# Optimization experiments

Measured on AMD Instinct MI355X. Metric: run time of the kernel, lower is better.

The kernel has to match this reference:

```python
import jax, jax.numpy as jnp
import numpy as np

B, C, L = 8, 512, 2048


def setup_inputs() -> dict:
    key = jax.random.key(0)
    ks = jax.random.split(key, 7)
    s = 1.0 / np.sqrt(C)
    return {
        "x": jax.random.normal(ks[0], (B, C, L), dtype=jnp.float32),
        "Wq": jax.random.normal(ks[1], (C, C), dtype=jnp.float32) * s,
        "bq": jax.random.normal(ks[2], (C,), dtype=jnp.float32) * s,
        "Wk": jax.random.normal(ks[3], (C, C), dtype=jnp.float32) * s,
        "bk": jax.random.normal(ks[4], (C,), dtype=jnp.float32) * s,
        "Wv": jax.random.normal(ks[5], (C, C), dtype=jnp.float32) * s,
        "bv": jax.random.normal(ks[6], (C,), dtype=jnp.float32) * s,
    }


def reference(x, Wq, bq, Wk, bk, Wv, bv):
    # Conv1d(kernel_size=1) == per-position linear: [C_out, C_in] @ x[b,:,l]
    q = jnp.einsum('oi,bil->bol', Wq, x) + bq[None, :, None]  # [B, C, L]
    k = jnp.einsum('oi,bil->bol', Wk, x) + bk[None, :, None]
    v = jnp.einsum('oi,bil->bol', Wv, x) + bv[None, :, None]
    scale = 1.0 / jnp.sqrt(jnp.asarray(x.shape[1], dtype=x.dtype))
    # scores[b, l, m] = sum_c q[b,c,l] * k[b,c,m] / sqrt(C)
    scores = jnp.einsum('bcl,bcm->blm', q, k) * scale  # [B, L, L]
    attn = jax.nn.softmax(scores, axis=-1)
    # out[b, c, l] = sum_m v[b,c,m] * attn[b,l,m]   (== bmm(V, attn^T))
    return jnp.einsum('bcm,blm->bcl', v, attn)  # [B, C, L]
```

## Files before the change

### kernel.cpp

```cpp
#include <hip/hip_runtime.h>
#include <hip/hip_bf16.h>
#include <math.h>

#define B 8
#define C 512
#define L 2048

using bf16x8 = __bf16 __attribute__((ext_vector_type(8)));
using f32x4  = float __attribute__((ext_vector_type(4)));

#define MFMA(a, b, c) __builtin_amdgcn_mfma_f32_16x16x32_bf16((a), (b), (c), 0, 0, 0)
#define SC2 0.06375872f
#define SH2 -17.312340f

__device__ __forceinline__ unsigned short f2bf(float f) {
    unsigned int u; __builtin_memcpy(&u, &f, 4);
    u += 0x7FFF + ((u >> 16) & 1);
    return (unsigned short)(u >> 16);
}
__device__ __forceinline__ void load_lds16(const unsigned short* g, unsigned short* l) {
    __builtin_amdgcn_global_load_lds(
        (const __attribute__((address_space(1))) unsigned int*)g,
        (__attribute__((address_space(3))) unsigned int*)l, 16, 0, 0);
}

template<int MODE, int KDIM>
__device__ __forceinline__ void gemm_core(
    const unsigned short* __restrict__ A,
    const unsigned short* __restrict__ Bm,
    unsigned short* As, unsigned short* Bs,
    void* __restrict__ OutV, int ldo,
    float* __restrict__ ep)
{
    const int t = threadIdx.x;
    const int wave = t >> 6, lane = t & 63;
    const int ll = t & 15, quad = (t >> 4) & 3;
    const int lr = lane >> 2, chunk = lane & 3;
    const int wm = (wave & 1) * 64, wn = (wave >> 1) * 64;

    const unsigned short* gA0 = A  + (size_t)(wave * 32 + lr) * KDIM + chunk * 8;
    const unsigned short* gB0 = Bm + (size_t)(wave * 32 + lr) * KDIM + chunk * 8;
    unsigned short* lA0 = As + (wave * 32) * 32;
    unsigned short* lB0 = Bs + (wave * 32) * 32;
    const int P1 = 128 * 32;

    f32x4 acc[4][4];
#pragma unroll
    for (int i = 0; i < 4; ++i)
#pragma unroll
        for (int j = 0; j < 4; ++j) acc[i][j] = (f32x4){0.f, 0.f, 0.f, 0.f};

#pragma unroll 1
    for (int k0 = 0; k0 < KDIM; k0 += 64) {
        __syncthreads();
        load_lds16(gA0 + k0, lA0);
        load_lds16(gA0 + (size_t)16 * KDIM + k0, lA0 + 16 * 32);
        load_lds16(gA0 + k0 + 32, lA0 + P1);
        load_lds16(gA0 + (size_t)16 * KDIM + k0 + 32, lA0 + P1 + 16 * 32);
        load_lds16(gB0 + k0, lB0);
        load_lds16(gB0 + (size_t)16 * KDIM + k0, lB0 + 16 * 32);
        load_lds16(gB0 + k0 + 32, lB0 + P1);
        load_lds16(gB0 + (size_t)16 * KDIM + k0 + 32, lB0 + P1 + 16 * 32);
        __syncthreads();

#pragma unroll
        for (int p = 0; p < 2; ++p) {
            bf16x8 af[4], bf[4];
#pragma unroll
            for (int mi = 0; mi < 4; ++mi)
                af[mi] = *(const bf16x8*)&As[p * P1 + (wm + mi * 16 + ll) * 32 + quad * 8];
#pragma unroll
            for (int ni = 0; ni < 4; ++ni)
                bf[ni] = *(const bf16x8*)&Bs[p * P1 + (wn + ni * 16 + ll) * 32 + quad * 8];
#pragma unroll
            for (int mi = 0; mi < 4; ++mi)
#pragma unroll
                for (int ni = 0; ni < 4; ++ni)
                    acc[mi][ni] = MFMA(af[mi], bf[ni], acc[mi][ni]);
        }
    }

#pragma unroll
    for (int mi = 0; mi < 4; ++mi)
#pragma unroll
        for (int ni = 0; ni < 4; ++ni) {
            const int col = wn + ni * 16 + ll;
            float epc = 0.f;
            if (MODE == 0) epc = ep[col];
            if (MODE == 3) epc = 1.0f / ep[col];
#pragma unroll
            for (int r = 0; r < 4; ++r) {
                const int row = wm + mi * 16 + quad * 4 + r;
                float v = acc[mi][ni][r];
                if (MODE == 0)      v += epc;
                else if (MODE == 1) v += ep[row];
                else                v *= epc;
                if (MODE == 3)
                    ((float*)OutV)[(size_t)row * ldo + col] = v;
                else
                    ((unsigned short*)OutV)[(size_t)row * ldo + col] = f2bf(v);
            }
        }
}

__global__ __launch_bounds__(256) void prep(
    const float* __restrict__ x, const float* __restrict__ Wq,
    const float* __restrict__ Wk, const float* __restrict__ Wv,
    unsigned short* __restrict__ xt, unsigned short* __restrict__ o,
    float* __restrict__ rsum)
{
    __shared__ float tile[64][69];
    const int t = threadIdx.x;
    const int flat = blockIdx.x + 32 * (blockIdx.y + 8 * blockIdx.z);

    if (flat < 768) {
        if (flat < 16) {
            float4 z = make_float4(0.f, 0.f, 0.f, 0.f);
            *(float4*)(rsum + (flat * 256 + t) * 4) = z;
        }
        const int i = (flat * 256 + t) * 4;
        const int which = i >> 18;
        const int off = i & 0x3FFFF;
        const float* src = (which == 0) ? Wq : (which == 1) ? Wk : Wv;
        float4 v = *(const float4*)(src + off);
        union { unsigned short h[4]; uint2 u; } pk;
        pk.h[0] = f2bf(v.x); pk.h[1] = f2bf(v.y); pk.h[2] = f2bf(v.z); pk.h[3] = f2bf(v.w);
        *(uint2*)(o + i) = pk.u;
    }

    const int b = blockIdx.z, l0 = blockIdx.x * 64, c0 = blockIdx.y * 64;
    const int lx = t & 15, cy = t >> 4;
    const float* xb = x + (size_t)b * C * L;
#pragma unroll
    for (int p = 0; p < 4; ++p) {
        float4 v = *(const float4*)(xb + (size_t)(c0 + p * 16 + cy) * L + l0 + lx * 4);
        tile[p * 16 + cy][lx * 4 + 0] = v.x;
        tile[p * 16 + cy][lx * 4 + 1] = v.y;
        tile[p * 16 + cy][lx * 4 + 2] = v.z;
        tile[p * 16 + cy][lx * 4 + 3] = v.w;
    }
    __syncthreads();
    const int ocl = t & 15, ot = t >> 4;
    unsigned short* xtb = xt + (size_t)b * L * C;
#pragma unroll
    for (int p = 0; p < 4; ++p) {
        int ol = p * 16 + ot;
        union { unsigned short h[4]; uint2 u; } pk;
#pragma unroll
        for (int i = 0; i < 4; ++i) pk.h[i] = f2bf(tile[ocl * 4 + i][ol]);
        *(uint2*)(xtb + (size_t)(l0 + ol) * C + c0 + ocl * 4) = pk.u;
    }
}

__global__ __launch_bounds__(256) void qkv_gemm(
    const unsigned short* __restrict__ xt, const unsigned short* __restrict__ Wb,
    const float* __restrict__ bq, const float* __restrict__ bk,
    const float* __restrict__ bv,
    unsigned short* __restrict__ Qt, unsigned short* __restrict__ Kt,
    unsigned short* __restrict__ Vv)
{
    __shared__ unsigned short As[2 * 128 * 32], Bs[2 * 128 * 32];
    const int id = blockIdx.x;
    const int b = id & 7, r = id >> 3;
    const int which = r >> 6, tt = r & 63;
    const unsigned short* xtb = xt + (size_t)b * L * C;
    if (which < 2) {
        const int m0 = (tt & 15) * 128, n0 = (tt >> 4) * 128;
        const unsigned short* A  = xtb + (size_t)m0 * C;
        const unsigned short* Bm = Wb + (size_t)which * C * C + (size_t)n0 * C;
        unsigned short* Out = (which ? Kt : Qt) + (size_t)b * L * C
                              + (size_t)m0 * C + n0;
        gemm_core<0, C>(A, Bm, As, Bs, Out, C,
                        const_cast<float*>((which ? bk : bq) + n0));
    } else {
        const int m0 = (tt & 3) * 128, n0 = (tt >> 2) * 128;
        const unsigned short* A  = Wb + (size_t)2 * C * C + (size_t)m0 * C;
        const unsigned short* Bm = xtb + (size_t)n0 * C;
        unsigned short* Out = Vv + (size_t)b * C * L + (size_t)m0 * L + n0;
        gemm_core<1, C>(A, Bm, As, Bs, Out, L, const_cast<float*>(bv + m0));
    }
}

__global__ __launch_bounds__(512, 4) void sc_exp3(
    const unsigned short* __restrict__ Qt, const unsigned short* __restrict__ Kt,
    unsigned short* __restrict__ P, float* __restrict__ rsum,
    int hoff, int qrows, int mshift)
{
    __shared__ unsigned short As[256 * 64];
    __shared__ unsigned short Bs[128 * 64];
    constexpr int KD = C;

    const int id = blockIdx.x;
    const int b = id & 7, rr = id >> 3;
    const int m0 = (rr & ((1 << mshift) - 1)) * 256, n0 = (rr >> mshift) * 128;
    const unsigned short* A  = Qt + (size_t)b * L * C + (size_t)(hoff + m0) * C;
    const unsigned short* Bm = Kt + (size_t)b * L * C + (size_t)n0 * C;
    unsigned short* Out = P + (size_t)b * qrows * L + (size_t)m0 * L + n0;
    float* ep = rsum + (size_t)b * L + hoff + m0;

    const int t = threadIdx.x;
    const int wave = t >> 6;
    const int ll = t & 15, quad = (t >> 4) & 3;
    const int wm = (wave & 3) * 64, wn = (wave >> 2) * 64;

    const int r0 = t >> 3;
    const int swz = ((t & 7) ^ (r0 & 7)) * 8;
    const unsigned short* gA = A  + (size_t)r0 * KD + swz;
    const unsigned short* gB = Bm + (size_t)r0 * KD + swz;
    unsigned short* lA = As + wave * 512;
    unsigned short* lB = Bs + wave * 512;
    const int sw8 = ll & 7;

    f32x4 acc[4][4];
#pragma unroll
    for (int i = 0; i < 4; ++i)
#pragma unroll
        for (int j = 0; j < 4; ++j) acc[i][j] = (f32x4){0.f, 0.f, 0.f, 0.f};

#pragma unroll 1
    for (int k0 = 0; k0 < KD; k0 += 64) {
        __syncthreads();
        load_lds16(gA + k0,                     lA);
        load_lds16(gA + (size_t)64  * KD + k0,  lA + 64 * 64);
        load_lds16(gA + (size_t)128 * KD + k0,  lA + 128 * 64);
        load_lds16(gA + (size_t)192 * KD + k0,  lA + 192 * 64);
        load_lds16(gB + k0,                     lB);
        load_lds16(gB + (size_t)64  * KD + k0,  lB + 64 * 64);
        __syncthreads();

#pragma unroll
        for (int p = 0; p < 2; ++p) {
            bf16x8 af[4], bf[4];
#pragma unroll
            for (int mi = 0; mi < 4; ++mi)
                af[mi] = *(const bf16x8*)&As[(wm + mi * 16 + ll) * 64
                                             + ((p * 4 + quad) ^ sw8) * 8];
#pragma unroll
            for (int ni = 0; ni < 4; ++ni)
                bf[ni] = *(const bf16x8*)&Bs[(wn + ni * 16 + ll) * 64
                                             + ((p * 4 + quad) ^ sw8) * 8];
#pragma unroll
            for (int mi = 0; mi < 4; ++mi)
#pragma unroll
                for (int ni = 0; ni < 4; ++ni)
                    acc[mi][ni] = MFMA(af[mi], bf[ni], acc[mi][ni]);
        }
    }

    float rpart[4][4];
#pragma unroll
    for (int mi = 0; mi < 4; ++mi)
#pragma unroll
        for (int r = 0; r < 4; ++r) rpart[mi][r] = 0.f;

#pragma unroll
    for (int mi = 0; mi < 4; ++mi)
#pragma unroll
        for (int ni = 0; ni < 4; ++ni) {
            const int col = wn + ni * 16 + ll;
#pragma unroll
            for (int r = 0; r < 4; ++r) {
                const int row = wm + mi * 16 + quad * 4 + r;
                float v = exp2f(fmaf(acc[mi][ni][r], SC2, SH2));
                rpart[mi][r] += v;
                Out[(size_t)row * L + col] = f2bf(v);
            }
        }
#pragma unroll
    for (int mi = 0; mi < 4; ++mi)
#pragma unroll
        for (int r = 0; r < 4; ++r) {
            float s = rpart[mi][r];
            s += __shfl_xor(s, 1, 64);
            s += __shfl_xor(s, 2, 64);
            s += __shfl_xor(s, 4, 64);
            s += __shfl_xor(s, 8, 64);
            if (ll == 0) atomicAdd(ep + wm + mi * 16 + quad * 4 + r, s);
        }
}

__global__ __launch_bounds__(512, 4) void pv_gemm2(
    const unsigned short* __restrict__ Vv, const unsigned short* __restrict__ P,
    const float* __restrict__ rsum, float* __restrict__ out)
{
    __shared__ unsigned short As[128 * 64];
    __shared__ unsigned short Bs[256 * 64];

    const int id = blockIdx.x;
    const int b = id & 7, rr = id >> 3;
    const int m0 = (rr & 3) * 128, n0 = (rr >> 2) * 256;
    const unsigned short* A  = Vv + (size_t)b * C * L + (size_t)m0 * L;
    const unsigned short* Bm = P  + (size_t)b * L * L + (size_t)n0 * L;
    float* Out = out + (size_t)b * C * L + (size_t)m0 * L + n0;
    const float* ep = rsum + (size_t)b * L + n0;

    const int t = threadIdx.x;
    const int wave = t >> 6;
    const int ll = t & 15, quad = (t >> 4) & 3;
    const int wm = (wave & 1) * 64, wn = (wave >> 1) * 64;

    const int r0 = t >> 3;
    const int swz = ((t & 7) ^ (r0 & 7)) * 8;
    const unsigned short* gA = A  + (size_t)r0 * L + swz;
    const unsigned short* gB = Bm + (size_t)r0 * L + swz;
    unsigned short* lA = As + wave * 512;
    unsigned short* lB = Bs + wave * 512;
    const int sw8 = ll & 7;

    f32x4 acc[4][4];
#pragma unroll
    for (int i = 0; i < 4; ++i)
#pragma unroll
        for (int j = 0; j < 4; ++j) acc[i][j] = (f32x4){0.f, 0.f, 0.f, 0.f};

#pragma unroll 1
    for (int k0 = 0; k0 < L; k0 += 64) {
        __syncthreads();
        load_lds16(gA + k0,                    lA);
        load_lds16(gA + (size_t)64  * L + k0,  lA + 64 * 64);
        load_lds16(gB + k0,                    lB);
        load_lds16(gB + (size_t)64  * L + k0,  lB + 64 * 64);
        load_lds16(gB + (size_t)128 * L + k0,  lB + 128 * 64);
        load_lds16(gB + (size_t)192 * L + k0,  lB + 192 * 64);
        __syncthreads();

#pragma unroll
        for (int p = 0; p < 2; ++p) {
            bf16x8 af[4], bf[4];
#pragma unroll
            for (int mi = 0; mi < 4; ++mi)
                af[mi] = *(const bf16x8*)&As[(wm + mi * 16 + ll) * 64
                                             + ((p * 4 + quad) ^ sw8) * 8];
#pragma unroll
            for (int ni = 0; ni < 4; ++ni)
                bf[ni] = *(const bf16x8*)&Bs[(wn + ni * 16 + ll) * 64
                                             + ((p * 4 + quad) ^ sw8) * 8];
#pragma unroll
            for (int mi = 0; mi < 4; ++mi)
#pragma unroll
                for (int ni = 0; ni < 4; ++ni)
                    acc[mi][ni] = MFMA(af[mi], bf[ni], acc[mi][ni]);
        }
    }

#pragma unroll
    for (int mi = 0; mi < 4; ++mi)
#pragma unroll
        for (int ni = 0; ni < 4; ++ni) {
            const int col = wn + ni * 16 + ll;
            const float inv = 1.0f / ep[col];
#pragma unroll
            for (int r = 0; r < 4; ++r) {
                const int row = wm + mi * 16 + quad * 4 + r;
                Out[(size_t)row * L + col] = acc[mi][ni][r] * inv;
            }
        }
}

__global__ __launch_bounds__(256) void pv_gemm(
    const unsigned short* __restrict__ Vv, const unsigned short* __restrict__ P,
    const float* __restrict__ rsum, float* __restrict__ out,
    int hoff, int qrows)
{
    __shared__ unsigned short As[2 * 128 * 32], Bs[2 * 128 * 32];
    const int id = blockIdx.x;
    const int b = id & 7, r = id >> 3;
    const int m0 = (r & 3) * 128, n0 = (r >> 2) * 128;
    const unsigned short* A  = Vv + (size_t)b * C * L + (size_t)m0 * L;
    const unsigned short* Bm = P + (size_t)b * qrows * L + (size_t)n0 * L;
    float* Out = out + (size_t)b * C * L + (size_t)m0 * L + hoff + n0;
    float* ep = const_cast<float*>(rsum) + (size_t)b * L + hoff + n0;
    gemm_core<3, L>(A, Bm, As, Bs, Out, L, ep);
}

extern "C" void kernel_launch(void* const* d_in, const int* in_sizes, int n_in,
                              void* d_out, int out_size, void* d_ws, size_t ws_size,
                              hipStream_t stream) {
    const float* x  = (const float*)d_in[0];
    const float* Wq = (const float*)d_in[1];
    const float* bq = (const float*)d_in[2];
    const float* Wk = (const float*)d_in[3];
    const float* bk = (const float*)d_in[4];
    const float* Wv = (const float*)d_in[5];
    const float* bv = (const float*)d_in[6];
    float* out = (float*)d_out;

    const size_t BCL = (size_t)B * C * L;
    const bool fullP = ws_size >= 119078912ull;

    unsigned short* Qt = (unsigned short*)d_ws;
    unsigned short* Kt = Qt + BCL;
    unsigned short* Vv = Kt + BCL;
    unsigned short *Wb, *xt, *P;
    float* rsum;
    if (fullP) {
        Wb   = Vv + BCL;
        rsum = (float*)(Wb + (size_t)3 * C * C);
        xt   = (unsigned short*)(rsum + (size_t)B * L);
        P    = xt;
    } else {
        xt   = Vv + BCL;
        P    = xt;
        Wb   = P + (size_t)B * 1024 * L;
        rsum = (float*)(Wb + (size_t)3 * C * C);
    }

    prep<<<dim3(L / 64, C / 64, B), 256, 0, stream>>>(x, Wq, Wk, Wv, xt, Wb, rsum);
    qkv_gemm<<<dim3(1536), 256, 0, stream>>>(xt, Wb, bq, bk, bv, Qt, Kt, Vv);

    if (fullP) {
        sc_exp3<<<dim3(1024), 512, 0, stream>>>(Qt, Kt, P, rsum, 0, L, 3);
        pv_gemm2<<<dim3(256), 512, 0, stream>>>(Vv, P, rsum, out);
    } else {
        for (int h = 0; h < 2; ++h) {
            sc_exp3<<<dim3(512), 512, 0, stream>>>(Qt, Kt, P, rsum, h * 1024, 1024, 2);
            pv_gemm<<<dim3(256), 256, 0, stream>>>(Vv, P, rsum, out, h * 1024, 1024);
        }
    }
}
```

Baseline: 221.4 us.

## Double-buffer LDS in score and PV GEMMs with smaller 128x128 tiles

```diff
diff --git a/kernel.cpp b/kernel.cpp
--- a/kernel.cpp
+++ b/kernel.cpp
@@ -12,6 +12,8 @@
 #define MFMA(a, b, c) __builtin_amdgcn_mfma_f32_16x16x32_bf16((a), (b), (c), 0, 0, 0)
 #define SC2 0.06375872f
 #define SH2 -17.312340f
+#define LGKMC(n) do { asm volatile("s_waitcnt lgkmcnt(" #n ")" ::: "memory"); \
+                      __builtin_amdgcn_sched_barrier(0); } while (0)
 
 __device__ __forceinline__ unsigned short f2bf(float f) {
     unsigned int u; __builtin_memcpy(&u, &f, 4);
@@ -22,6 +24,87 @@
     __builtin_amdgcn_global_load_lds(
         (const __attribute__((address_space(1))) unsigned int*)g,
         (__attribute__((address_space(3))) unsigned int*)l, 16, 0, 0);
+}
+__device__ __forceinline__ bf16x8 dsr128(unsigned byteoff) {
+    bf16x8 r;
+    asm volatile("ds_read_b128 %0, %1" : "=v"(r) : "v"(byteoff));
+    return r;
+}
+
+template<int KDIM>
+__device__ __forceinline__ void dbuf_gemm128(
+    const unsigned short* __restrict__ gA, int lda,
+    const unsigned short* __restrict__ gB, int ldb,
+    unsigned short* AsBase, unsigned short* BsBase,
+    f32x4 (&acc)[4][2])
+{
+    const int t = threadIdx.x;
+    const int wave = t >> 6;
+    const int ll = t & 15, quad = (t >> 4) & 3;
+    const int wm = (wave & 1) * 64, wn = (wave >> 1) * 32;
+    const int sw8 = ll & 7;
+    const unsigned c0b = (unsigned)((quad ^ sw8) * 16);
+    const unsigned c1b = (unsigned)(((4 + quad) ^ sw8) * 16);
+    const unsigned ldsA = (unsigned)(unsigned long long)AsBase;
+    const unsigned ldsB = (unsigned)(unsigned long long)BsBase;
+    const unsigned aOff = (unsigned)((wm + ll) * 128);
+    const unsigned bOff = (unsigned)((wn + ll) * 128);
+    unsigned short* lA = AsBase + wave * 512;
+    unsigned short* lB = BsBase + wave * 512;
+    constexpr int NT = KDIM / 64;
+
+    load_lds16(gA,                    lA);
+    load_lds16(gA + (size_t)64 * lda, lA + 4096);
+    load_lds16(gB,                    lB);
+    load_lds16(gB + (size_t)64 * ldb, lB + 4096);
+    __syncthreads();
+
+    int cur = 0;
+#pragma unroll 1
+    for (int kt = 0; kt < NT; ++kt) {
+        if (kt + 1 < NT) {
+            const int k1 = (kt + 1) * 64;
+            unsigned short* sA = lA + (cur ^ 1) * 8192;
+            unsigned short* sB = lB + (cur ^ 1) * 8192;
+            load_lds16(gA + k1,                    sA);
+            load_lds16(gA + (size_t)64 * lda + k1, sA + 4096);
+            load_lds16(gB + k1,                    sB);
+            load_lds16(gB + (size_t)64 * ldb + k1, sB + 4096);
+        }
+        const unsigned aAdr = ldsA + (unsigned)(cur * 16384) + aOff;
+        const unsigned bAdr = ldsB + (unsigned)(cur * 16384) + bOff;
+        bf16x8 a0[4], b0[2], a1[4], b1[2];
+        a0[0] = dsr128(aAdr + 0 * 2048 + c0b);
+        a0[1] = dsr128(aAdr + 1 * 2048 + c0b);
+        a0[2] = dsr128(aAdr + 2 * 2048 + c0b);
+        a0[3] = dsr128(aAdr + 3 * 2048 + c0b);
+        b0[0] = dsr128(bAdr + 0 * 2048 + c0b);
+        b0[1] = dsr128(bAdr + 1 * 2048 + c0b);
+        a1[0] = dsr128(aAdr + 0 * 2048 + c1b);
+        a1[1] = dsr128(aAdr + 1 * 2048 + c1b);
+        a1[2] = dsr128(aAdr + 2 * 2048 + c1b);
+        a1[3] = dsr128(aAdr + 3 * 2048 + c1b);
+        b1[0] = dsr128(bAdr + 0 * 2048 + c1b);
+        b1[1] = dsr128(bAdr + 1 * 2048 + c1b);
+        LGKMC(6);
+        __builtin_amdgcn_s_setprio(1);
+#pragma unroll
+        for (int mi = 0; mi < 4; ++mi)
+#pragma unroll
+            for (int ni = 0; ni < 2; ++ni)
+                acc[mi][ni] = MFMA(a0[mi], b0[ni], acc[mi][ni]);
+        __builtin_amdgcn_s_setprio(0);
+        LGKMC(0);
+        __builtin_amdgcn_s_setprio(1);
+#pragma unroll
+        for (int mi = 0; mi < 4; ++mi)
+#pragma unroll
+            for (int ni = 0; ni < 2; ++ni)
+                acc[mi][ni] = MFMA(a1[mi], b1[ni], acc[mi][ni]);
+        __builtin_amdgcn_s_setprio(0);
+        __syncthreads();
+        cur ^= 1;
+    }
 }
 
 template<int MODE, int KDIM>
@@ -181,71 +264,37 @@
     }
 }
 
-__global__ __launch_bounds__(512, 4) void sc_exp3(
+__global__ __launch_bounds__(512, 4) void sc_exp4(
     const unsigned short* __restrict__ Qt, const unsigned short* __restrict__ Kt,
     unsigned short* __restrict__ P, float* __restrict__ rsum,
     int hoff, int qrows, int mshift)
 {
-    __shared__ unsigned short As[256 * 64];
-    __shared__ unsigned short Bs[128 * 64];
-    constexpr int KD = C;
-
+    __shared__ unsigned short As[2][8192], Bs[2][8192];
     const int id = blockIdx.x;
     const int b = id & 7, rr = id >> 3;
-    const int m0 = (rr & ((1 << mshift) - 1)) * 256, n0 = (rr >> mshift) * 128;
-    const unsigned short* A  = Qt + (size_t)b * L * C + (size_t)(hoff + m0) * C;
-    const unsigned short* Bm = Kt + (size_t)b * L * C + (size_t)n0 * C;
+    const int m0 = (rr & ((1 << mshift) - 1)) * 128, n0 = (rr >> mshift) * 128;
+
+    const int t = threadIdx.x;
+    const int r0 = t >> 3;
+    const int swz = ((t & 7) ^ (r0 & 7)) * 8;
+    const unsigned short* gA = Qt + (size_t)b * L * C
+                               + (size_t)(hoff + m0 + r0) * C + swz;
+    const unsigned short* gB = Kt + (size_t)b * L * C
+                               + (size_t)(n0 + r0) * C + swz;
+
+    f32x4 acc[4][2];
+#pragma unroll
+    for (int i = 0; i < 4; ++i)
+#pragma unroll
+        for (int j = 0; j < 2; ++j) acc[i][j] = (f32x4){0.f, 0.f, 0.f, 0.f};
+
+    dbuf_gemm128<C>(gA, C, gB, C, &As[0][0], &Bs[0][0], acc);
+
     unsigned short* Out = P + (size_t)b * qrows * L + (size_t)m0 * L + n0;
     float* ep = rsum + (size_t)b * L + hoff + m0;
-
-    const int t = threadIdx.x;
     const int wave = t >> 6;
     const int ll = t & 15, quad = (t >> 4) & 3;
-    const int wm = (wave & 3) * 64, wn = (wave >> 2) * 64;
-
-    const int r0 = t >> 3;
-    const int swz = ((t & 7) ^ (r0 & 7)) * 8;
-    const unsigned short* gA = A  + (size_t)r0 * KD + swz;
-    const unsigned short* gB = Bm + (size_t)r0 * KD + swz;
-    unsigned short* lA = As + wave * 512;
-    unsigned short* lB = Bs + wave * 512;
-    const int sw8 = ll & 7;
-
-    f32x4 acc[4][4];
-#pragma unroll
-    for (int i = 0; i < 4; ++i)
-#pragma unroll
-        for (int j = 0; j < 4; ++j) acc[i][j] = (f32x4){0.f, 0.f, 0.f, 0.f};
-
-#pragma unroll 1
-    for (int k0 = 0; k0 < KD; k0 += 64) {
-        __syncthreads();
-        load_lds16(gA + k0,                     lA);
-        load_lds16(gA + (size_t)64  * KD + k0,  lA + 64 * 64);
-        load_lds16(gA + (size_t)128 * KD + k0,  lA + 128 * 64);
-        load_lds16(gA + (size_t)192 * KD + k0,  lA + 192 * 64);
-        load_lds16(gB + k0,                     lB);
-        load_lds16(gB + (size_t)64  * KD + k0,  lB + 64 * 64);
-        __syncthreads();
-
-#pragma unroll
-        for (int p = 0; p < 2; ++p) {
-            bf16x8 af[4], bf[4];
-#pragma unroll
-            for (int mi = 0; mi < 4; ++mi)
-                af[mi] = *(const bf16x8*)&As[(wm + mi * 16 + ll) * 64
-                                             + ((p * 4 + quad) ^ sw8) * 8];
-#pragma unroll
-            for (int ni = 0; ni < 4; ++ni)
-                bf[ni] = *(const bf16x8*)&Bs[(wn + ni * 16 + ll) * 64
-                                             + ((p * 4 + quad) ^ sw8) * 8];
-#pragma unroll
-            for (int mi = 0; mi < 4; ++mi)
-#pragma unroll
-                for (int ni = 0; ni < 4; ++ni)
-                    acc[mi][ni] = MFMA(af[mi], bf[ni], acc[mi][ni]);
-        }
-    }
+    const int wm = (wave & 1) * 64, wn = (wave >> 1) * 32;
 
     float rpart[4][4];
 #pragma unroll
@@ -256,7 +305,7 @@
 #pragma unroll
     for (int mi = 0; mi < 4; ++mi)
 #pragma unroll
-        for (int ni = 0; ni < 4; ++ni) {
+        for (int ni = 0; ni < 2; ++ni) {
             const int col = wn + ni * 16 + ll;
 #pragma unroll
             for (int r = 0; r < 4; ++r) {
@@ -279,74 +328,41 @@
         }
 }
 
-__global__ __launch_bounds__(512, 4) void pv_gemm2(
+__global__ __launch_bounds__(512, 4) void pv_gemm3(
     const unsigned short* __restrict__ Vv, const unsigned short* __restrict__ P,
     const float* __restrict__ rsum, float* __restrict__ out)
 {
-    __shared__ unsigned short As[128 * 64];
-    __shared__ unsigned short Bs[256 * 64];
-
+    __shared__ unsigned short As[2][8192], Bs[2][8192];
     const int id = blockIdx.x;
     const int b = id & 7, rr = id >> 3;
-    const int m0 = (rr & 3) * 128, n0 = (rr >> 2) * 256;
-    const unsigned short* A  = Vv + (size_t)b * C * L + (size_t)m0 * L;
-    const unsigned short* Bm = P  + (size_t)b * L * L + (size_t)n0 * L;
+    const int m0 = (rr & 3) * 128, n0 = (rr >> 2) * 128;
+
+    const int t = threadIdx.x;
+    const int r0 = t >> 3;
+    const int swz = ((t & 7) ^ (r0 & 7)) * 8;
+    const unsigned short* gA = Vv + (size_t)b * C * L
+                               + (size_t)(m0 + r0) * L + swz;
+    const unsigned short* gB = P + (size_t)b * L * L
+                               + (size_t)(n0 + r0) * L + swz;
+
+    f32x4 acc[4][2];
+#pragma unroll
+    for (int i = 0; i < 4; ++i)
+#pragma unroll
+        for (int j = 0; j < 2; ++j) acc[i][j] = (f32x4){0.f, 0.f, 0.f, 0.f};
+
+    dbuf_gemm128<L>(gA, L, gB, L, &As[0][0], &Bs[0][0], acc);
+
     float* Out = out + (size_t)b * C * L + (size_t)m0 * L + n0;
     const float* ep = rsum + (size_t)b * L + n0;
-
-    const int t = threadIdx.x;
     const int wave = t >> 6;
     const int ll = t & 15, quad = (t >> 4) & 3;
-    const int wm = (wave & 1) * 64, wn = (wave >> 1) * 64;
-
-    const int r0 = t >> 3;
-    const int swz = ((t & 7) ^ (r0 & 7)) * 8;
-    const unsigned short* gA = A  + (size_t)r0 * L + swz;
-    const unsigned short* gB = Bm + (size_t)r0 * L + swz;
-    unsigned short* lA = As + wave * 512;
-    unsigned short* lB = Bs + wave * 512;
-    const int sw8 = ll & 7;
-
-    f32x4 acc[4][4];
-#pragma unroll
-    for (int i = 0; i < 4; ++i)
-#pragma unroll
-        for (int j = 0; j < 4; ++j) acc[i][j] = (f32x4){0.f, 0.f, 0.f, 0.f};
-
-#pragma unroll 1
-    for (int k0 = 0; k0 < L; k0 += 64) {
-        __syncthreads();
-        load_lds16(gA + k0,                    lA);
-        load_lds16(gA + (size_t)64  * L + k0,  lA + 64 * 64);
-        load_lds16(gB + k0,                    lB);
-        load_lds16(gB + (size_t)64  * L + k0,  lB + 64 * 64);
-        load_lds16(gB + (size_t)128 * L + k0,  lB + 128 * 64);
-        load_lds16(gB + (size_t)192 * L + k0,  lB + 192 * 64);
-        __syncthreads();
-
-#pragma unroll
-        for (int p = 0; p < 2; ++p) {
-            bf16x8 af[4], bf[4];
-#pragma unroll
-            for (int mi = 0; mi < 4; ++mi)
-                af[mi] = *(const bf16x8*)&As[(wm + mi * 16 + ll) * 64
-                                             + ((p * 4 + quad) ^ sw8) * 8];
-#pragma unroll
-            for (int ni = 0; ni < 4; ++ni)
-                bf[ni] = *(const bf16x8*)&Bs[(wn + ni * 16 + ll) * 64
-                                             + ((p * 4 + quad) ^ sw8) * 8];
-#pragma unroll
-            for (int mi = 0; mi < 4; ++mi)
-#pragma unroll
-                for (int ni = 0; ni < 4; ++ni)
-                    acc[mi][ni] = MFMA(af[mi], bf[ni], acc[mi][ni]);
-        }
-    }
+    const int wm = (wave & 1) * 64, wn = (wave >> 1) * 32;
 
 #pragma unroll
     for (int mi = 0; mi < 4; ++mi)
 #pragma unroll
-        for (int ni = 0; ni < 4; ++ni) {
+        for (int ni = 0; ni < 2; ++ni) {
             const int col = wn + ni * 16 + ll;
             const float inv = 1.0f / ep[col];
 #pragma unroll
@@ -409,11 +425,11 @@
     qkv_gemm<<<dim3(1536), 256, 0, stream>>>(xt, Wb, bq, bk, bv, Qt, Kt, Vv);
 
     if (fullP) {
-        sc_exp3<<<dim3(1024), 512, 0, stream>>>(Qt, Kt, P, rsum, 0, L, 3);
-        pv_gemm2<<<dim3(256), 512, 0, stream>>>(Vv, P, rsum, out);
+        sc_exp4<<<dim3(2048), 512, 0, stream>>>(Qt, Kt, P, rsum, 0, L, 4);
+        pv_gemm3<<<dim3(512), 512, 0, stream>>>(Vv, P, rsum, out);
     } else {
         for (int h = 0; h < 2; ++h) {
-            sc_exp3<<<dim3(512), 512, 0, stream>>>(Qt, Kt, P, rsum, h * 1024, 1024, 2);
+            sc_exp4<<<dim3(1024), 512, 0, stream>>>(Qt, Kt, P, rsum, h * 1024, 1024, 3);
             pv_gemm<<<dim3(256), 256, 0, stream>>>(Vv, P, rsum, out, h * 1024, 1024);
         }
     }
```

Result: faster. 212.8 us (-3.9%).
